# Kernel optimization log

Measured on AMD Instinct MI355X. Metric: run time of the kernel, lower is better.

Reference implementation:

```python
import jax, jax.numpy as jnp
import numpy as np
from jax import lax

H = 128  # LSTM hidden size (hardcoded in module)

def setup_inputs() -> dict:
    key = jax.random.key(0)
    ks = jax.random.split(key, 10)
    B, S, D = 256, 512, 80
    T = 3
    s_in = 1.0 / np.sqrt(D)
    s_h = 1.0 / np.sqrt(H)
    return {
        "x": jax.random.normal(ks[0], (B, S, D), dtype=jnp.float32),
        "W_in": jax.random.uniform(ks[1], (256, D), jnp.float32, -s_in, s_in),
        "b_in": jax.random.uniform(ks[2], (256,), jnp.float32, -s_in, s_in),
        "W_ih": jax.random.uniform(ks[3], (4 * H, 256), jnp.float32, -s_h, s_h),
        "b_ih": jax.random.uniform(ks[4], (4 * H,), jnp.float32, -s_h, s_h),
        "W_hh": jax.random.uniform(ks[5], (4 * H, H), jnp.float32, -s_h, s_h),
        "b_hh": jax.random.uniform(ks[6], (4 * H,), jnp.float32, -s_h, s_h),
        "w_time": jax.random.uniform(ks[7], (T,), jnp.float32, -1.0 / np.sqrt(T), 1.0 / np.sqrt(T)),
        "W_br": jax.random.uniform(ks[8], (4, H), jnp.float32, -s_h, s_h),
        "b_br": jax.random.uniform(ks[9], (4,), jnp.float32, -s_h, s_h),
        "batch_size": B,
        "time_steps": T,
    }


def reference(x, W_in, b_in, W_ih, b_ih, W_hh, b_hh, w_time, W_br, b_br, batch_size, time_steps):
    # input projection (dropout is identity in eval mode)
    xl = jnp.einsum('bsd,ed->bse', x, W_in) + b_in  # [B,S,256]
    B, S, _ = xl.shape
    T = time_steps

    def step(carry, inp):
        h, c, h_st, c_st = carry
        xt, i = inp  # xt: [B,256], i: step index
        gates = xt @ W_ih.T + b_ih + h @ W_hh.T + b_hh  # [B,4H]
        ig, fg, gg, og = jnp.split(gates, 4, axis=-1)
        c_new = jax.nn.sigmoid(fg) * c + jax.nn.sigmoid(ig) * jnp.tanh(gg)
        h_new = jax.nn.sigmoid(og) * jnp.tanh(c_new)
        slot = i % T
        oh = jax.nn.one_hot(slot, T, dtype=h_new.dtype)  # [T]
        h_st = h_st * (1.0 - oh) + h_new[:, :, None] * oh  # [B,H,T]
        c_st = c_st * (1.0 - oh) + c_new[:, :, None] * oh
        pool = (slot == T - 1)
        ph = jnp.einsum('bht,t->bh', h_st, w_time)
        pc = jnp.einsum('bht,t->bh', c_st, w_time)
        h_out = jnp.where(pool, ph, h_new)
        c_out = jnp.where(pool, pc, c_new)
        h_st = jnp.where(pool, jnp.zeros_like(h_st), h_st)
        c_st = jnp.where(pool, jnp.zeros_like(c_st), c_st)
        return (h_out, c_out, h_st, c_st), h_out

    init = (jnp.zeros((B, H), xl.dtype), jnp.zeros((B, H), xl.dtype),
            jnp.zeros((B, H, T), xl.dtype), jnp.zeros((B, H, T), xl.dtype))
    _, outs = lax.scan(step, init, (jnp.swapaxes(xl, 0, 1), jnp.arange(S)))
    out = jnp.swapaxes(outs, 0, 1)  # [B,S,H]
    logits = jnp.einsum('bsh,oh->bso', out, W_br) + b_br  # [B,S,4]
    return jax.nn.log_softmax(logits, axis=2)
```

## Files before the change

kernel.cpp:

```cpp
#include <hip/hip_runtime.h>
#include <hip/hip_fp16.h>

#define BB 256
#define SS 512
#define DD 80
#define HH 128
#define GG 512

typedef _Float16 h2_t __attribute__((ext_vector_type(2)));
typedef _Float16 half8 __attribute__((ext_vector_type(8)));
typedef float f32x4 __attribute__((ext_vector_type(4)));

union U32H2 { unsigned int u; h2_t h; unsigned short us[2]; };

static __device__ __forceinline__ h2_t u2h(unsigned int u) { U32H2 x; x.u = u; return x.h; }

static __device__ __forceinline__ unsigned int pk2(float a, float b) {
  unsigned int lo = (unsigned int)__half_as_ushort(__float2half(a));
  unsigned int hi = (unsigned int)__half_as_ushort(__float2half(b));
  return (hi << 16) | lo;
}

static __device__ __forceinline__ float fdot2(unsigned int a, unsigned int b, float c) {
#if __has_builtin(__builtin_amdgcn_fdot2)
  return __builtin_amdgcn_fdot2(u2h(a), u2h(b), c, false);
#else
  U32H2 ua, ub; ua.u = a; ub.u = b;
  return c + (float)ua.h[0] * (float)ub.h[0] + (float)ua.h[1] * (float)ub.h[1];
#endif
}

static __device__ __forceinline__ float fsig(float x) {
  return __fdividef(1.f, 1.f + __expf(-x));
}

__global__ __launch_bounds__(128) void prep_kernel(
    const float* __restrict__ W_in, const float* __restrict__ b_in,
    const float* __restrict__ W_ih, const float* __restrict__ b_ih,
    const float* __restrict__ W_hh, const float* __restrict__ b_hh,
    unsigned short* __restrict__ wc16, unsigned short* __restrict__ whh16,
    float* __restrict__ biasc)
{
  const int g = blockIdx.x;
  const int t = threadIdx.x;
  const float* wih = W_ih + g * 256;
  if (t < DD) {
    float s = 0.f;
    for (int e = 0; e < 256; ++e) s += wih[e] * W_in[e * DD + t];
    wc16[g * DD + t] = __half_as_ushort(__float2half(s));
  }
  whh16[g * HH + t] = __half_as_ushort(__float2half(W_hh[g * HH + t]));
  if (t == 0) {
    float s = 0.f;
    for (int e = 0; e < 256; ++e) s += wih[e] * b_in[e];
    biasc[g] = s + b_ih[g] + b_hh[g];
  }
}

__global__ __launch_bounds__(256) void gemm_kernel(
    const float* __restrict__ x,
    const unsigned int* __restrict__ wc,
    uint4* __restrict__ gx)
{
  __shared__ unsigned int Al[64 * 52];
  __shared__ unsigned int Bl[128 * 52];
  const int t  = threadIdx.x;
  const int mt = blockIdx.x;
  const int g0 = blockIdx.y * 128;

  {
    const float4* xr = (const float4*)(x + (size_t)mt * 64 * DD);
    #pragma unroll
    for (int i = 0; i < 5; ++i) {
      int f = t + i * 256;
      int row = f / 20, c4 = f % 20;
      float4 v = xr[row * 20 + c4];
      Al[row * 52 + c4 * 2]     = pk2(v.x, v.y);
      Al[row * 52 + c4 * 2 + 1] = pk2(v.z, v.w);
    }
    #pragma unroll
    for (int i = 0; i < 3; ++i) {
      int f = t + i * 256;
      int row = f / 12, c = f % 12;
      Al[row * 52 + 40 + c] = 0u;
    }
  }
  {
    #pragma unroll
    for (int i = 0; i < 5; ++i) {
      int f = t + i * 256;
      int row = f / 10, c4 = f % 10;
      uint4 v = *(const uint4*)(wc + (size_t)(g0 + row) * 40 + c4 * 4);
      *(uint4*)&Bl[row * 52 + c4 * 4] = v;
    }
    #pragma unroll
    for (int i = 0; i < 3; ++i) {
      int f = t + i * 256;
      int row = f / 12, c = f % 12;
      Bl[row * 52 + 40 + c] = 0u;
    }
  }
  __syncthreads();

  const int w = t >> 6, lane = t & 63;
  const int m = lane & 15, q = lane >> 4;

  half8 af[3];
  #pragma unroll
  for (int kk = 0; kk < 3; ++kk)
    af[kk] = *(const half8*)((const char*)Al + (size_t)(w * 16 + m) * 208 + kk * 64 + q * 16);

  #pragma unroll
  for (int j = 0; j < 8; ++j) {
    f32x4 acc = {0.f, 0.f, 0.f, 0.f};
    #pragma unroll
    for (int kk = 0; kk < 3; ++kk) {
      half8 bf = *(const half8*)((const char*)Bl + (size_t)(j * 16 + m) * 208 + kk * 64 + q * 16);
      acc = __builtin_amdgcn_mfma_f32_16x16x32_f16(af[kk], bf, acc, 0, 0, 0);
    }
    unsigned int lo  = pk2(acc[0], acc[1]);
    unsigned int hi  = pk2(acc[2], acc[3]);
    unsigned int plo = (unsigned int)__shfl_down((int)lo, 16);
    unsigned int phi = (unsigned int)__shfl_down((int)hi, 16);
    if ((q & 1) == 0) {
      uint4 o; o.x = lo; o.y = hi; o.z = plo; o.w = phi;
      gx[((size_t)mt * 8 + w * 2 + (q >> 1)) * 512 + (size_t)(g0 + j * 16 + m)] = o;
    }
  }
}

__global__ __attribute__((amdgpu_waves_per_eu(1, 1))) __launch_bounds__(256)
void scan_kernel(
    const uint4* __restrict__ gx,
    const uint4* __restrict__ whh,
    const float* __restrict__ biasc,
    const float* __restrict__ wtime,
    __half* __restrict__ hout)
{
  __shared__ unsigned int hbuf[2][64];
  const int b    = blockIdx.x;
  const int t    = threadIdx.x;
  const int lane = t & 63;
  const int hi   = t >> 1;
  const int odd  = t & 1;
  const int g1   = odd * 128 + hi;
  const int g2   = g1 + 256;

  unsigned int w1[64], w2[64];
  {
    const uint4* wr1 = whh + (size_t)g1 * 16;
    const uint4* wr2 = whh + (size_t)g2 * 16;
    #pragma unroll
    for (int i = 0; i < 16; ++i) {
      uint4 v = wr1[i];
      w1[4*i] = v.x; w1[4*i+1] = v.y; w1[4*i+2] = v.z; w1[4*i+3] = v.w;
      uint4 u = wr2[i];
      w2[4*i] = u.x; w2[4*i+1] = u.y; w2[4*i+2] = u.z; w2[4*i+3] = u.w;
    }
  }
  const float bias1 = biasc[g1];
  const float bias2 = biasc[g2];
  const float wt0 = wtime[0], wt1 = wtime[1], wt2 = wtime[2];
  if (t < 64) { hbuf[0][t] = 0u; hbuf[1][t] = 0u; }
  float c = 0.f, hst0 = 0.f, hst1 = 0.f, cst0 = 0.f, cst1 = 0.f;
  int slot = 0, s = 0;
  const uint4* gxp1 = gx + (size_t)b * 64 * 512 + g1;
  const uint4* gxp2 = gx + (size_t)b * 64 * 512 + g2;
  __syncthreads();

  uint4 gv1 = gxp1[0];
  uint4 gv2 = gxp2[0];
  for (int sb = 0; sb < 64; ++sb) {
    uint4 gn1, gn2;
    if (sb < 63) {
      gn1 = gxp1[(size_t)(sb + 1) * 512];
      gn2 = gxp2[(size_t)(sb + 1) * 512];
    }
    unsigned int ga1[4] = {gv1.x, gv1.y, gv1.z, gv1.w};
    unsigned int ga2[4] = {gv2.x, gv2.y, gv2.z, gv2.w};
    #pragma unroll
    for (int i = 0; i < 8; ++i) {
      const int par = s & 1;
      const unsigned int hreg = hbuf[par][lane];
      U32H2 u1; u1.u = ga1[i >> 1];
      U32H2 u2; u2.u = ga2[i >> 1];
      const float gxi1 = (float)u1.h[i & 1];
      const float gxi2 = (float)u2.h[i & 1];
      float d1a = bias1 + gxi1, d1b = 0.f;
      float d2a = bias2 + gxi2, d2b = 0.f;
      #pragma unroll
      for (int p = 0; p < 64; p += 2) {
        unsigned int h0 = (unsigned int)__builtin_amdgcn_readlane((int)hreg, p);
        unsigned int h1 = (unsigned int)__builtin_amdgcn_readlane((int)hreg, p + 1);
        d1a = fdot2(w1[p],     h0, d1a);
        d2a = fdot2(w2[p],     h0, d2a);
        d1b = fdot2(w1[p + 1], h1, d1b);
        d2b = fdot2(w2[p + 1], h1, d2b);
      }
      const float d1 = d1a + d1b;
      const float d2 = d2a + d2b;
      const float a1 = fsig(d1);
      const float yin = odd ? d2 : (d2 + d2);
      const float sv  = fsig(yin);
      const float a2  = odd ? sv : (2.f * sv - 1.f);
      const float p1 = __shfl_xor(a1, 1);
      const float p2 = __shfl_xor(a2, 1);
      const float iv = odd ? p1 : a1;
      const float gg = odd ? p2 : a2;
      const float fv = odd ? a1 : p1;
      const float ov = odd ? a2 : p2;
      c = fv * c + iv * gg;
      const float tc = 2.f * fsig(c + c) - 1.f;
      const float hn = ov * tc;
      float hcur;
      if (slot == 2) {
        hcur = hst0 * wt0 + hst1 * wt1 + hn * wt2;
        c    = cst0 * wt0 + cst1 * wt1 + c  * wt2;
        slot = 0;
      } else {
        hcur = hn;
        if (slot == 0) { hst0 = hn; cst0 = c; }
        else           { hst1 = hn; cst1 = c; }
        ++slot;
      }
      if (!odd) {
        const __half hh = __float2half(hcur);
        ((__half*)hbuf[par ^ 1])[hi] = hh;
        hout[((size_t)b * SS + s) * HH + hi] = hh;
      }
      ++s;
      __syncthreads();
    }
    gv1 = gn1;
    gv2 = gn2;
  }
}

__global__ __launch_bounds__(256) void out_kernel(
    const uint4* __restrict__ hout,
    const float* __restrict__ Wbr, const float* __restrict__ bbr,
    float4* __restrict__ out)
{
  __shared__ unsigned int wb[4][64];
  __shared__ float bbs[4];
  const int t = threadIdx.x;
  {
    const int o = t >> 6, p = t & 63;
    wb[o][p] = pk2(Wbr[o * HH + 2 * p], Wbr[o * HH + 2 * p + 1]);
  }
  if (t < 4) bbs[t] = bbr[t];
  __syncthreads();

  const size_t row = (size_t)blockIdx.x * 256 + t;
  const uint4* hr = hout + row * 16;
  float a0 = bbs[0], a1 = bbs[1], a2 = bbs[2], a3 = bbs[3];
  #pragma unroll
  for (int q = 0; q < 16; ++q) {
    uint4 hv = hr[q];
    unsigned int hd[4] = {hv.x, hv.y, hv.z, hv.w};
    #pragma unroll
    for (int d = 0; d < 4; ++d) {
      const int p = q * 4 + d;
      a0 = fdot2(hd[d], wb[0][p], a0);
      a1 = fdot2(hd[d], wb[1][p], a1);
      a2 = fdot2(hd[d], wb[2][p], a2);
      a3 = fdot2(hd[d], wb[3][p], a3);
    }
  }
  const float m = fmaxf(fmaxf(a0, a1), fmaxf(a2, a3));
  const float e0 = __expf(a0 - m), e1 = __expf(a1 - m), e2 = __expf(a2 - m), e3 = __expf(a3 - m);
  const float lse = m + __logf(e0 + e1 + e2 + e3);
  out[row] = make_float4(a0 - lse, a1 - lse, a2 - lse, a3 - lse);
}

extern "C" void kernel_launch(void* const* d_in, const int* in_sizes, int n_in,
                              void* d_out, int out_size, void* d_ws, size_t ws_size,
                              hipStream_t stream) {
  const float* x     = (const float*)d_in[0];
  const float* W_in  = (const float*)d_in[1];
  const float* b_in  = (const float*)d_in[2];
  const float* W_ih  = (const float*)d_in[3];
  const float* b_ih  = (const float*)d_in[4];
  const float* W_hh  = (const float*)d_in[5];
  const float* b_hh  = (const float*)d_in[6];
  const float* wtime = (const float*)d_in[7];
  const float* W_br  = (const float*)d_in[8];
  const float* b_br  = (const float*)d_in[9];
  (void)in_sizes; (void)n_in; (void)out_size; (void)ws_size;

  char* ws = (char*)d_ws;
  unsigned short* wc16  = (unsigned short*)(ws + 0);
  unsigned short* whh16 = (unsigned short*)(ws + 81920);
  float*          biasc = (float*)(ws + 212992);
  __half*         hout  = (__half*)(ws + 215040);
  uint4*          gx    = (uint4*)(ws + 33769472);

  prep_kernel<<<512, 128, 0, stream>>>(W_in, b_in, W_ih, b_ih, W_hh, b_hh,
                                       wc16, whh16, biasc);
  gemm_kernel<<<dim3(2048, 4), 256, 0, stream>>>(x, (const unsigned int*)wc16, gx);
  scan_kernel<<<256, 256, 0, stream>>>(gx, (const uint4*)whh16, biasc, wtime, hout);
  out_kernel<<<512, 256, 0, stream>>>((const uint4*)hout, W_br, b_br, (float4*)d_out);
}
```

Measured before the change: 559.9 us.

## Split LSTM scan across 512 threads with one gate row per thread

The recurrent scan kernel moves from 256 threads, each computing two gate rows, to 512 threads, each computing one gate row. The four gates of a hidden unit are exchanged between adjacent lanes with xor shuffles. The GEMM kernel writes gx columns in an interleaved order so each scan thread reads one contiguous uint4 per step. This halves the serial dot-product length and register weight footprint per thread, but the per-step barrier now spans more waves and adds more shuffles. The GEMM's zero-fill loop count also changes from 3 to 6.

```diff
diff --git a/kernel.cpp b/kernel.cpp
--- a/kernel.cpp
+++ b/kernel.cpp
@@ -94,7 +94,7 @@
       *(uint4*)&Bl[row * 52 + c4 * 4] = v;
     }
     #pragma unroll
-    for (int i = 0; i < 3; ++i) {
+    for (int i = 0; i < 6; ++i) {
       int f = t + i * 256;
       int row = f / 12, c = f % 12;
       Bl[row * 52 + 40 + c] = 0u;
@@ -123,13 +123,15 @@
     unsigned int plo = (unsigned int)__shfl_down((int)lo, 16);
     unsigned int phi = (unsigned int)__shfl_down((int)hi, 16);
     if ((q & 1) == 0) {
+      const int gl  = g0 + j * 16 + m;
+      const int col = ((gl & 127) << 2) | (gl >> 7);
       uint4 o; o.x = lo; o.y = hi; o.z = plo; o.w = phi;
-      gx[((size_t)mt * 8 + w * 2 + (q >> 1)) * 512 + (size_t)(g0 + j * 16 + m)] = o;
-    }
-  }
-}
-
-__global__ __attribute__((amdgpu_waves_per_eu(1, 1))) __launch_bounds__(256)
+      gx[((size_t)mt * 8 + w * 2 + (q >> 1)) * 512 + (size_t)col] = o;
+    }
+  }
+}
+
+__global__ __attribute__((amdgpu_waves_per_eu(2, 2))) __launch_bounds__(512)
 void scan_kernel(
     const uint4* __restrict__ gx,
     const uint4* __restrict__ whh,
@@ -141,74 +143,62 @@
   const int b    = blockIdx.x;
   const int t    = threadIdx.x;
   const int lane = t & 63;
-  const int hi   = t >> 1;
-  const int odd  = t & 1;
-  const int g1   = odd * 128 + hi;
-  const int g2   = g1 + 256;
-
-  unsigned int w1[64], w2[64];
-  {
-    const uint4* wr1 = whh + (size_t)g1 * 16;
-    const uint4* wr2 = whh + (size_t)g2 * 16;
+  const int q    = t & 3;
+  const int hi2  = t >> 2;
+  const int g    = q * 128 + hi2;
+
+  unsigned int w[64];
+  {
+    const uint4* wr = whh + (size_t)g * 16;
     #pragma unroll
     for (int i = 0; i < 16; ++i) {
-      uint4 v = wr1[i];
-      w1[4*i] = v.x; w1[4*i+1] = v.y; w1[4*i+2] = v.z; w1[4*i+3] = v.w;
-      uint4 u = wr2[i];
-      w2[4*i] = u.x; w2[4*i+1] = u.y; w2[4*i+2] = u.z; w2[4*i+3] = u.w;
-    }
-  }
-  const float bias1 = biasc[g1];
-  const float bias2 = biasc[g2];
+      uint4 v = wr[i];
+      w[4*i] = v.x; w[4*i+1] = v.y; w[4*i+2] = v.z; w[4*i+3] = v.w;
+    }
+  }
+  const float bias = biasc[g];
   const float wt0 = wtime[0], wt1 = wtime[1], wt2 = wtime[2];
   if (t < 64) { hbuf[0][t] = 0u; hbuf[1][t] = 0u; }
   float c = 0.f, hst0 = 0.f, hst1 = 0.f, cst0 = 0.f, cst1 = 0.f;
   int slot = 0, s = 0;
-  const uint4* gxp1 = gx + (size_t)b * 64 * 512 + g1;
-  const uint4* gxp2 = gx + (size_t)b * 64 * 512 + g2;
+  const uint4* gxp = gx + (size_t)b * 64 * 512 + t;
   __syncthreads();
 
-  uint4 gv1 = gxp1[0];
-  uint4 gv2 = gxp2[0];
+  uint4 gv = gxp[0];
   for (int sb = 0; sb < 64; ++sb) {
-    uint4 gn1, gn2;
-    if (sb < 63) {
-      gn1 = gxp1[(size_t)(sb + 1) * 512];
-      gn2 = gxp2[(size_t)(sb + 1) * 512];
-    }
-    unsigned int ga1[4] = {gv1.x, gv1.y, gv1.z, gv1.w};
-    unsigned int ga2[4] = {gv2.x, gv2.y, gv2.z, gv2.w};
+    uint4 gn = gv;
+    if (sb < 63) gn = gxp[(size_t)(sb + 1) * 512];
+    unsigned int ga[4] = {gv.x, gv.y, gv.z, gv.w};
     #pragma unroll
     for (int i = 0; i < 8; ++i) {
       const int par = s & 1;
       const unsigned int hreg = hbuf[par][lane];
-      U32H2 u1; u1.u = ga1[i >> 1];
-      U32H2 u2; u2.u = ga2[i >> 1];
-      const float gxi1 = (float)u1.h[i & 1];
-      const float gxi2 = (float)u2.h[i & 1];
-      float d1a = bias1 + gxi1, d1b = 0.f;
-      float d2a = bias2 + gxi2, d2b = 0.f;
+      U32H2 gu; gu.u = ga[i >> 1];
+      const float gxi = (float)gu.h[i & 1];
+      float d0 = bias + gxi, d1 = 0.f, d2 = 0.f, d3 = 0.f;
       #pragma unroll
-      for (int p = 0; p < 64; p += 2) {
-        unsigned int h0 = (unsigned int)__builtin_amdgcn_readlane((int)hreg, p);
-        unsigned int h1 = (unsigned int)__builtin_amdgcn_readlane((int)hreg, p + 1);
-        d1a = fdot2(w1[p],     h0, d1a);
-        d2a = fdot2(w2[p],     h0, d2a);
-        d1b = fdot2(w1[p + 1], h1, d1b);
-        d2b = fdot2(w2[p + 1], h1, d2b);
+      for (int p = 0; p < 64; p += 4) {
+        int h0 = __builtin_amdgcn_readlane((int)hreg, p);
+        int h1 = __builtin_amdgcn_readlane((int)hreg, p + 1);
+        int h2 = __builtin_amdgcn_readlane((int)hreg, p + 2);
+        int h3 = __builtin_amdgcn_readlane((int)hreg, p + 3);
+        d0 = fdot2(w[p],     (unsigned int)h0, d0);
+        d1 = fdot2(w[p + 1], (unsigned int)h1, d1);
+        d2 = fdot2(w[p + 2], (unsigned int)h2, d2);
+        d3 = fdot2(w[p + 3], (unsigned int)h3, d3);
       }
-      const float d1 = d1a + d1b;
-      const float d2 = d2a + d2b;
-      const float a1 = fsig(d1);
-      const float yin = odd ? d2 : (d2 + d2);
-      const float sv  = fsig(yin);
-      const float a2  = odd ? sv : (2.f * sv - 1.f);
-      const float p1 = __shfl_xor(a1, 1);
-      const float p2 = __shfl_xor(a2, 1);
-      const float iv = odd ? p1 : a1;
-      const float gg = odd ? p2 : a2;
-      const float fv = odd ? a1 : p1;
-      const float ov = odd ? a2 : p2;
+      const float d = (d0 + d1) + (d2 + d3);
+      const float din = (q == 2) ? d + d : d;
+      const float sv  = fsig(din);
+      const float a   = (q == 2) ? 2.f * sv - 1.f : sv;
+      const float v1 = __shfl_xor(a, 1);
+      const float v2 = __shfl_xor(a, 2);
+      const float v3 = __shfl_xor(a, 3);
+      const int b0 = q & 1, b1 = q >> 1;
+      const float iv = b1 ? (b0 ? v3 : v2) : (b0 ? v1 : a);
+      const float fv = b1 ? (b0 ? v2 : v3) : (b0 ? a  : v1);
+      const float gg = b1 ? (b0 ? v1 : a ) : (b0 ? v3 : v2);
+      const float ov = b1 ? (b0 ? a  : v1) : (b0 ? v2 : v3);
       c = fv * c + iv * gg;
       const float tc = 2.f * fsig(c + c) - 1.f;
       const float hn = ov * tc;
@@ -223,16 +213,15 @@
         else           { hst1 = hn; cst1 = c; }
         ++slot;
       }
-      if (!odd) {
-        const __half hh = __float2half(hcur);
-        ((__half*)hbuf[par ^ 1])[hi] = hh;
-        hout[((size_t)b * SS + s) * HH + hi] = hh;
+      if (q == 0) {
+        const __half hh2 = __float2half(hcur);
+        ((__half*)hbuf[par ^ 1])[hi2] = hh2;
+        hout[((size_t)b * SS + s) * HH + hi2] = hh2;
       }
       ++s;
       __syncthreads();
     }
-    gv1 = gn1;
-    gv2 = gn2;
+    gv = gn;
   }
 }
 
@@ -255,12 +244,12 @@
   const uint4* hr = hout + row * 16;
   float a0 = bbs[0], a1 = bbs[1], a2 = bbs[2], a3 = bbs[3];
   #pragma unroll
-  for (int q = 0; q < 16; ++q) {
-    uint4 hv = hr[q];
+  for (int qq = 0; qq < 16; ++qq) {
+    uint4 hv = hr[qq];
     unsigned int hd[4] = {hv.x, hv.y, hv.z, hv.w};
     #pragma unroll
     for (int d = 0; d < 4; ++d) {
-      const int p = q * 4 + d;
+      const int p = qq * 4 + d;
       a0 = fdot2(hd[d], wb[0][p], a0);
       a1 = fdot2(hd[d], wb[1][p], a1);
       a2 = fdot2(hd[d], wb[2][p], a2);
@@ -298,6 +287,6 @@
   prep_kernel<<<512, 128, 0, stream>>>(W_in, b_in, W_ih, b_ih, W_hh, b_hh,
                                        wc16, whh16, biasc);
   gemm_kernel<<<dim3(2048, 4), 256, 0, stream>>>(x, (const unsigned int*)wc16, gx);
-  scan_kernel<<<256, 256, 0, stream>>>(gx, (const uint4*)whh16, biasc, wtime, hout);
+  scan_kernel<<<256, 512, 0, stream>>>(gx, (const uint4*)whh16, biasc, wtime, hout);
   out_kernel<<<512, 256, 0, stream>>>((const uint4*)hout, W_br, b_br, (float4*)d_out);
 }
```

Measured after the change: 684.8 us. +22.3%, slower.
